# Optimization experiments

Hardware: AMD Instinct MI355X
Metric: run time of the kernel (lower is better)

## Reference

```python
import jax, jax.numpy as jnp
import numpy as np

N = 262144
E_COLS, E_ROWS = 4, 4
E = E_COLS * E_ROWS
HID = 20
N_IN, N_OUT = 2, 1
COLS = jnp.array([-4.0, -0.674, 0.0, 0.674, 4.0], dtype=jnp.float32)
ROWS = jnp.array([-4.0, -0.674, 0.0, 0.674, 4.0], dtype=jnp.float32)


def setup_inputs() -> dict:
    key = jax.random.key(0)
    ks = jax.random.split(key, 11)
    s = lambda fan_in: 1.0 / np.sqrt(fan_in)
    return {
        "x": jax.random.normal(ks[0], (N, N_IN), dtype=jnp.float32),
        "W1": jax.random.normal(ks[1], (E, N_IN, HID), dtype=jnp.float32) * s(N_IN),
        "b1": jnp.zeros((E, HID), dtype=jnp.float32),
        "W2": jax.random.normal(ks[2], (E, HID, HID), dtype=jnp.float32) * s(HID),
        "b2": jnp.zeros((E, HID), dtype=jnp.float32),
        "W3": jax.random.normal(ks[3], (E, HID, HID), dtype=jnp.float32) * s(HID),
        "b3": jnp.zeros((E, HID), dtype=jnp.float32),
        "W4": jax.random.normal(ks[4], (E, HID, HID), dtype=jnp.float32) * s(HID),
        "b4": jnp.zeros((E, HID), dtype=jnp.float32),
        "W5": jax.random.normal(ks[5], (E, HID, N_OUT), dtype=jnp.float32) * s(HID),
        "b5": jnp.zeros((E, N_OUT), dtype=jnp.float32),
    }


def _region_mask(v, bounds):
    # v: [N], bounds: [K+1] -> bool [K, N]; lower bound inclusive only for first cell
    lb = bounds[:-1][:, None]
    ub = bounds[1:][:, None]
    lower = v[None, :] > lb
    lower = lower.at[0].set(v >= bounds[0])
    return lower & (v[None, :] <= ub)


def reference(x, W1, b1, W2, b2, W3, b3, W4, b4, W5, b5):
    xn = jax.lax.stop_gradient(x)  # indicator uses detached input
    cm = _region_mask(xn[:, 0], COLS)  # [4, N]
    rm = _region_mask(xn[:, 1], ROWS)  # [4, N]
    mask = (cm[:, None, :] & rm[None, :, :]).reshape(E, -1).astype(x.dtype)  # [E, N]

    silu = jax.nn.silu  # idrlnet MLP default activation = swish
    h = silu(jnp.einsum('nd,edh->enh', x, W1) + b1[:, None, :])   # [E, N, 20]
    h = silu(jnp.einsum('enh,ehk->enk', h, W2) + b2[:, None, :])
    h = silu(jnp.einsum('enh,ehk->enk', h, W3) + b3[:, None, :])
    h = silu(jnp.einsum('enh,ehk->enk', h, W4) + b4[:, None, :])
    out = jnp.einsum('enh,eho->eno', h, W5) + b5[:, None, :]      # [E, N, 1]

    # masked sum over experts: each sample lies in exactly one grid cell
    y = jnp.einsum('en,eno->no', mask, out)  # [N, 1]
    return y
```

## Files before the change

kernel.cpp:

```cpp
#include <hip/hip_runtime.h>

#define NTHREADS 1024

constexpr int HID    = 20;
constexpr int NEXP   = 16;
constexpr int ESTRIDE = 1348;

constexpr int OFF_W1 = 0;
constexpr int OFF_B1 = 40;
constexpr int OFF_W2 = 60;
constexpr int OFF_B2 = 460;
constexpr int OFF_W3 = 480;
constexpr int OFF_B3 = 880;
constexpr int OFF_W4 = 900;
constexpr int OFF_B4 = 1300;
constexpr int OFF_W5 = 1320;
constexpr int OFF_B5 = 1340;

__device__ __forceinline__ float silu(float v) {
    float e = __expf(-v);
    return v * __builtin_amdgcn_rcpf(1.0f + e);
}

__device__ __forceinline__ int cell_idx(float v) {
    if (!(v >= -4.0f))  return -1;
    if (v <= -0.674f)   return 0;
    if (v <= 0.0f)      return 1;
    if (v <= 0.674f)    return 2;
    if (v <= 4.0f)      return 3;
    return -1;
}

template<int PER_E>
__device__ __forceinline__ void stage(float* smem, const float* __restrict__ src,
                                      int off, int tid) {
    constexpr int TOTAL = NEXP * PER_E;
    for (int i = tid; i < TOTAL; i += NTHREADS) {
        int e = i / PER_E;
        int k = i - e * PER_E;
        smem[e * ESTRIDE + off + k] = src[i];
    }
}

__device__ __forceinline__ void layer20(float (&h)[HID],
                                        const float* __restrict__ Wm,
                                        const float* __restrict__ bv) {
    float acc[HID];
    const float4* bb = reinterpret_cast<const float4*>(bv);
    #pragma unroll
    for (int q = 0; q < 5; ++q) {
        float4 b = bb[q];
        acc[4*q+0] = b.x; acc[4*q+1] = b.y; acc[4*q+2] = b.z; acc[4*q+3] = b.w;
    }
    #pragma unroll
    for (int k = 0; k < HID; ++k) {
        const float hk = h[k];
        const float4* row = reinterpret_cast<const float4*>(Wm + k * HID);
        #pragma unroll
        for (int q = 0; q < 5; ++q) {
            float4 w = row[q];
            acc[4*q+0] = fmaf(hk, w.x, acc[4*q+0]);
            acc[4*q+1] = fmaf(hk, w.y, acc[4*q+1]);
            acc[4*q+2] = fmaf(hk, w.z, acc[4*q+2]);
            acc[4*q+3] = fmaf(hk, w.w, acc[4*q+3]);
        }
    }
    #pragma unroll
    for (int j = 0; j < HID; ++j) h[j] = silu(acc[j]);
}

__global__ __launch_bounds__(NTHREADS, 4) void NetEval_2207613190845_kernel(
    const float* __restrict__ x,
    const float* __restrict__ W1, const float* __restrict__ b1,
    const float* __restrict__ W2, const float* __restrict__ b2,
    const float* __restrict__ W3, const float* __restrict__ b3,
    const float* __restrict__ W4, const float* __restrict__ b4,
    const float* __restrict__ W5, const float* __restrict__ b5,
    float* __restrict__ out, int n_total)
{
    __shared__ float smem[NEXP * ESTRIDE];
    const int tid = threadIdx.x;

    stage<40 >(smem, W1, OFF_W1, tid);
    stage<20 >(smem, b1, OFF_B1, tid);
    stage<400>(smem, W2, OFF_W2, tid);
    stage<20 >(smem, b2, OFF_B2, tid);
    stage<400>(smem, W3, OFF_W3, tid);
    stage<20 >(smem, b3, OFF_B3, tid);
    stage<400>(smem, W4, OFF_W4, tid);
    stage<20 >(smem, b4, OFF_B4, tid);
    stage<20 >(smem, W5, OFF_W5, tid);
    stage<1  >(smem, b5, OFF_B5, tid);
    __syncthreads();

    const int n = blockIdx.x * NTHREADS + tid;
    if (n >= n_total) return;

    const float2 xv = reinterpret_cast<const float2*>(x)[n];
    const int c = cell_idx(xv.x);
    const int r = cell_idx(xv.y);

    float result = 0.0f;
    if ((c | r) >= 0) {
        const float* W = &smem[(c * 4 + r) * ESTRIDE];

        float h[HID];
        {
            const float4* w0 = reinterpret_cast<const float4*>(W + OFF_W1);
            const float4* w1 = reinterpret_cast<const float4*>(W + OFF_W1 + HID);
            const float4* bb = reinterpret_cast<const float4*>(W + OFF_B1);
            #pragma unroll
            for (int q = 0; q < 5; ++q) {
                float4 a0 = w0[q], a1 = w1[q], b = bb[q];
                h[4*q+0] = silu(fmaf(xv.x, a0.x, fmaf(xv.y, a1.x, b.x)));
                h[4*q+1] = silu(fmaf(xv.x, a0.y, fmaf(xv.y, a1.y, b.y)));
                h[4*q+2] = silu(fmaf(xv.x, a0.z, fmaf(xv.y, a1.z, b.z)));
                h[4*q+3] = silu(fmaf(xv.x, a0.w, fmaf(xv.y, a1.w, b.w)));
            }
        }
        layer20(h, W + OFF_W2, W + OFF_B2);
        layer20(h, W + OFF_W3, W + OFF_B3);
        layer20(h, W + OFF_W4, W + OFF_B4);
        float acc = W[OFF_B5];
        {
            const float4* w5 = reinterpret_cast<const float4*>(W + OFF_W5);
            #pragma unroll
            for (int q = 0; q < 5; ++q) {
                float4 w = w5[q];
                acc = fmaf(h[4*q+0], w.x, acc);
                acc = fmaf(h[4*q+1], w.y, acc);
                acc = fmaf(h[4*q+2], w.z, acc);
                acc = fmaf(h[4*q+3], w.w, acc);
            }
        }
        result = acc;
    }
    out[n] = result;
}

extern "C" void kernel_launch(void* const* d_in, const int* in_sizes, int n_in,
                              void* d_out, int out_size, void* d_ws, size_t ws_size,
                              hipStream_t stream) {
    const float* x  = (const float*)d_in[0];
    const float* W1 = (const float*)d_in[1];
    const float* b1 = (const float*)d_in[2];
    const float* W2 = (const float*)d_in[3];
    const float* b2 = (const float*)d_in[4];
    const float* W3 = (const float*)d_in[5];
    const float* b3 = (const float*)d_in[6];
    const float* W4 = (const float*)d_in[7];
    const float* b4 = (const float*)d_in[8];
    const float* W5 = (const float*)d_in[9];
    const float* b5 = (const float*)d_in[10];
    float* out = (float*)d_out;

    const int n_total = in_sizes[0] / 2;
    const int grid = (n_total + NTHREADS - 1) / NTHREADS;

    hipLaunchKernelGGL(NetEval_2207613190845_kernel, dim3(grid), dim3(NTHREADS), 0, stream,
                       x, W1, b1, W2, b2, W3, b3, W4, b4, W5, b5, out, n_total);
}
```

Measured before the change: 22.47 us.

## Sort samples by expert within each block to make wave weight reads uniform

Each block now ballots its samples by expert cell, builds per-wave and per-expert prefix offsets in shared memory, and scatters inputs into expert-sorted order. Threads in a wave therefore mostly read the same expert's weights from LDS, which turns scattered reads that conflict or diverge into broadcasts. Results are written back to their original index. Weight staging also moves to float4 copies. The cost is several extra barriers, 17 ballot rounds and extra shared memory per block, which may reduce occupancy.

```diff
diff --git a/kernel.cpp b/kernel.cpp
--- a/kernel.cpp
+++ b/kernel.cpp
@@ -4,6 +4,8 @@
 
 constexpr int HID    = 20;
 constexpr int NEXP   = 16;
+constexpr int NW     = NTHREADS / 64;
+constexpr int NB     = 17;
 constexpr int ESTRIDE = 1348;
 
 constexpr int OFF_W1 = 0;
@@ -31,9 +33,21 @@
     return -1;
 }
 
+template<int PER_E4>
+__device__ __forceinline__ void stage4(float* smem, const float* __restrict__ src,
+                                       int off, int tid) {
+    constexpr int TOTAL = NEXP * PER_E4;
+    const float4* s4 = reinterpret_cast<const float4*>(src);
+    for (int i = tid; i < TOTAL; i += NTHREADS) {
+        int e = i / PER_E4;
+        int k = i - e * PER_E4;
+        *reinterpret_cast<float4*>(&smem[e * ESTRIDE + off + 4 * k]) = s4[i];
+    }
+}
+
 template<int PER_E>
-__device__ __forceinline__ void stage(float* smem, const float* __restrict__ src,
-                                      int off, int tid) {
+__device__ __forceinline__ void stage1(float* smem, const float* __restrict__ src,
+                                       int off, int tid) {
     constexpr int TOTAL = NEXP * PER_E;
     for (int i = tid; i < TOTAL; i += NTHREADS) {
         int e = i / PER_E;
@@ -78,32 +92,77 @@
     const float* __restrict__ W5, const float* __restrict__ b5,
     float* __restrict__ out, int n_total)
 {
-    __shared__ float smem[NEXP * ESTRIDE];
+    __shared__ float  smem[NEXP * ESTRIDE];
+    __shared__ float2 sx[NTHREADS];
+    __shared__ int    sinfo[NTHREADS];
+    __shared__ int    wavecnt[NW * NB];
+    __shared__ int    waveoff[NW * NB];
+    __shared__ int    tot[NB];
+    __shared__ int    ebase[NB];
+
     const int tid = threadIdx.x;
 
-    stage<40 >(smem, W1, OFF_W1, tid);
-    stage<20 >(smem, b1, OFF_B1, tid);
-    stage<400>(smem, W2, OFF_W2, tid);
-    stage<20 >(smem, b2, OFF_B2, tid);
-    stage<400>(smem, W3, OFF_W3, tid);
-    stage<20 >(smem, b3, OFF_B3, tid);
-    stage<400>(smem, W4, OFF_W4, tid);
-    stage<20 >(smem, b4, OFF_B4, tid);
-    stage<20 >(smem, W5, OFF_W5, tid);
-    stage<1  >(smem, b5, OFF_B5, tid);
-    __syncthreads();
-
-    const int n = blockIdx.x * NTHREADS + tid;
-    if (n >= n_total) return;
-
-    const float2 xv = reinterpret_cast<const float2*>(x)[n];
+    stage4<10 >(smem, W1, OFF_W1, tid);
+    stage4<5  >(smem, b1, OFF_B1, tid);
+    stage4<100>(smem, W2, OFF_W2, tid);
+    stage4<5  >(smem, b2, OFF_B2, tid);
+    stage4<100>(smem, W3, OFF_W3, tid);
+    stage4<5  >(smem, b3, OFF_B3, tid);
+    stage4<100>(smem, W4, OFF_W4, tid);
+    stage4<5  >(smem, b4, OFF_B4, tid);
+    stage4<5  >(smem, W5, OFF_W5, tid);
+    stage1<1  >(smem, b5, OFF_B5, tid);
+
+    const int n  = blockIdx.x * NTHREADS + tid;
+    const int nc = n < n_total ? n : (n_total - 1);
+    const float2 xv = reinterpret_cast<const float2*>(x)[nc];
     const int c = cell_idx(xv.x);
     const int r = cell_idx(xv.y);
+    const int e = (n < n_total && (c | r) >= 0) ? (c * 4 + r) : 16;
+
+    const int lane = tid & 63;
+    const int wv   = tid >> 6;
+    unsigned long long mymask = 0ull;
+    #pragma unroll
+    for (int k = 0; k < NB; ++k) {
+        unsigned long long m = __ballot(e == k);
+        if (e == k) mymask = m;
+        if (lane == 0) wavecnt[wv * NB + k] = __popcll(m);
+    }
+    const int rank = __popcll(mymask & ((1ull << lane) - 1ull));
+    __syncthreads();
+
+    if (tid < NB) {
+        int run = 0;
+        #pragma unroll
+        for (int w = 0; w < NW; ++w) {
+            int cc = wavecnt[w * NB + tid];
+            waveoff[w * NB + tid] = run;
+            run += cc;
+        }
+        tot[tid] = run;
+    }
+    __syncthreads();
+    if (tid == 0) {
+        int run = 0;
+        #pragma unroll
+        for (int k = 0; k < NB; ++k) { ebase[k] = run; run += tot[k]; }
+    }
+    __syncthreads();
+
+    const int slot = ebase[e] + waveoff[wv * NB + e] + rank;
+    sx[slot]    = xv;
+    sinfo[slot] = tid | (e << 12);
+    __syncthreads();
+
+    const int    info = sinfo[tid];
+    const float2 xs   = sx[tid];
+    const int    es   = info >> 12;
+    const int    oidx = info & 0xFFF;
 
     float result = 0.0f;
-    if ((c | r) >= 0) {
-        const float* W = &smem[(c * 4 + r) * ESTRIDE];
-
+    if (es < 16) {
+        const float* W = &smem[es * ESTRIDE];
         float h[HID];
         {
             const float4* w0 = reinterpret_cast<const float4*>(W + OFF_W1);
@@ -112,10 +171,10 @@
             #pragma unroll
             for (int q = 0; q < 5; ++q) {
                 float4 a0 = w0[q], a1 = w1[q], b = bb[q];
-                h[4*q+0] = silu(fmaf(xv.x, a0.x, fmaf(xv.y, a1.x, b.x)));
-                h[4*q+1] = silu(fmaf(xv.x, a0.y, fmaf(xv.y, a1.y, b.y)));
-                h[4*q+2] = silu(fmaf(xv.x, a0.z, fmaf(xv.y, a1.z, b.z)));
-                h[4*q+3] = silu(fmaf(xv.x, a0.w, fmaf(xv.y, a1.w, b.w)));
+                h[4*q+0] = silu(fmaf(xs.x, a0.x, fmaf(xs.y, a1.x, b.x)));
+                h[4*q+1] = silu(fmaf(xs.x, a0.y, fmaf(xs.y, a1.y, b.y)));
+                h[4*q+2] = silu(fmaf(xs.x, a0.z, fmaf(xs.y, a1.z, b.z)));
+                h[4*q+3] = silu(fmaf(xs.x, a0.w, fmaf(xs.y, a1.w, b.w)));
             }
         }
         layer20(h, W + OFF_W2, W + OFF_B2);
@@ -135,7 +194,9 @@
         }
         result = acc;
     }
-    out[n] = result;
+
+    const int on = blockIdx.x * NTHREADS + oidx;
+    if (on < n_total) out[on] = result;
 }
 
 extern "C" void kernel_launch(void* const* d_in, const int* in_sizes, int n_in,
```

New measurement: 22.33 us. No clear change (-0.7%).
